# Optimization experiments

Hardware: AMD Instinct MI355X
Metric: run time of the kernel (lower is better)

The kernel has to match this reference:

```python
import jax, jax.numpy as jnp
import numpy as np
from jax import lax

LEADS = 61
BETA = 2.0
DN = ('NCHW', 'OIHW', 'NCHW')


def setup_inputs() -> dict:
    key = jax.random.key(0)
    ks = jax.random.split(key, 11)
    B, L = 128, LEADS
    w = lambda k, shape: jax.random.normal(k, shape, jnp.float32) * 0.1
    return {
        "x": jax.random.normal(ks[0], (B, L, 32, 250), jnp.float32),
        "w1": w(ks[1], (L, 8, 1, 3, 4)),   "b1": w(ks[2], (L, 8)),
        "w2": w(ks[3], (L, 16, 8, 4, 3)),  "b2": w(ks[4], (L, 16)),
        "w3": w(ks[5], (L, 32, 16, 3, 4)), "b3": w(ks[6], (L, 32)),
        "w4": w(ks[7], (L, 64, 32, 2, 4)), "b4": w(ks[8], (L, 64)),
        "fcw": w(ks[9], (L, 3, 64)),       "fcb": w(ks[10], (L, 3)),
    }


def _maxpool2(h):
    return lax.reduce_window(h, -jnp.inf, lax.max, (1, 1, 2, 2), (1, 1, 2, 2), 'VALID')


def _lead(x, w1, b1, w2, b2, w3, b3, w4, b4, fcw, fcb):
    # x: (B,1,32,250) for a single lead; weights for that lead only
    h = lax.conv_general_dilated(x, w1, (1, 2), [(1, 1), (2, 2)], dimension_numbers=DN) + b1[None, :, None, None]
    h = jax.nn.relu(_maxpool2(h))                                  # (B,8,16,63)
    h = lax.conv_general_dilated(h, w2, (2, 2), [(1, 1), (1, 1)], dimension_numbers=DN) + b2[None, :, None, None]
    h = jax.nn.relu(_maxpool2(h))                                  # (B,16,4,16)
    h = lax.conv_general_dilated(h, w3, (1, 2), [(1, 1), (1, 1)], dimension_numbers=DN) + b3[None, :, None, None]
    h = jax.nn.relu(_maxpool2(h))                                  # (B,32,2,4)
    h = lax.conv_general_dilated(h, w4, (1, 1), 'VALID', dimension_numbers=DN) + b4[None, :, None, None]  # (B,64,1,1)
    h = h.reshape(h.shape[0], 64)
    logits = h @ fcw.T + fcb                                       # (B,3)
    return jax.nn.softmax(logits, axis=-1)


def reference(x, w1, b1, w2, b2, w3, b3, w4, b4, fcw, fcb):
    # batch all 61 per-lead pipelines via vmap over the lead axis
    xl = jnp.transpose(x, (1, 0, 2, 3))[:, :, None]                # (L,B,1,32,250)
    preds = jax.vmap(_lead)(xl, w1, b1, w2, b2, w3, b3, w4, b4, fcw, fcb)  # (L,B,3)
    preds = jnp.transpose(preds, (1, 0, 2))                        # (B,L,3)
    # eval-mode multiplicative fusion loss (Liu et al.)
    one_m = 1.0 - preds
    prod_all = jnp.prod(one_m, axis=1, keepdims=True)              # prod over all leads
    coeff = lax.stop_gradient(prod_all / one_m)                    # prod over k != j (detached)
    beta_exp = BETA / (LEADS - 1)
    loss = -jnp.sum(coeff ** beta_exp * jnp.log(preds), axis=1)    # (B,3)
    return loss
```

## Files before the change

kernel.cpp:

```cpp
#include <hip/hip_runtime.h>
#include <math.h>
#include <utility>

#define NLEADS 61
#define AIL __attribute__((always_inline))

template <int... Is, typename F>
__device__ __forceinline__ void sf_(std::integer_sequence<int, Is...>, F&& f) {
    (f(std::integral_constant<int, Is>{}), ...);
}
template <int N, typename F>
__device__ __forceinline__ void static_for(F&& f) {
    sf_(std::make_integer_sequence<int, N>{}, (F&&)f);
}

__device__ __forceinline__ float4 ld4(const float* p) { return *(const float4*)p; }
__device__ __forceinline__ float2 ld2(const float* p) { return *(const float2*)p; }

template <int C> __device__ __forceinline__ float f4c(float4 v) {
    if constexpr (C == 0) return v.x;
    else if constexpr (C == 1) return v.y;
    else if constexpr (C == 2) return v.z;
    else return v.w;
}
template <int C> __device__ __forceinline__ float f6(float4 a, float2 b) {
    if constexpr (C < 4) return f4c<C>(a);
    else if constexpr (C == 4) return b.x;
    else return b.y;
}
template <int K> __device__ __forceinline__ float w12(float4 w0, float4 w1, float4 w2) {
    if constexpr (K < 4) return f4c<K>(w0);
    else if constexpr (K < 8) return f4c<K - 4>(w1);
    else return f4c<K - 8>(w2);
}

__global__ __launch_bounds__(256, 4)
void lead_cnn_kernel(const float* __restrict__ x,
                     const float* __restrict__ w1g, const float* __restrict__ b1g,
                     const float* __restrict__ w2g, const float* __restrict__ b2g,
                     const float* __restrict__ w3g, const float* __restrict__ b3g,
                     const float* __restrict__ w4g, const float* __restrict__ b4g,
                     const float* __restrict__ fcwg, const float* __restrict__ fcbg,
                     float* __restrict__ preds)
{
    __shared__ __align__(16) float smem[9992];
    float* const A  = smem;
    float* const H2 = smem + 8704;

    const int t = threadIdx.x;
    const int b = blockIdx.x;
    const int l = blockIdx.y;

    const float* xg  = x + ((size_t)b * NLEADS + l) * 8000;
    const float* w1l = w1g + l * 96;
    const float* b1l = b1g + l * 8;

    float acc1[32];
    static_for<4>([&](auto IT) AIL {
        constexpr int it = IT.value;
        const int item = t + it * 256;
        const int ph = item / 63;
        const int pw = item - ph * 63;
        const int c1 = (pw == 0) ? 0 : (4 * pw - 2);
        const int c3 = (pw >= 62) ? 248 : (4 * pw + 2);
        const bool lok = (pw > 0), rok = (pw < 62);
        float xw[24];
        static_for<4>([&](auto R) AIL {
            constexpr int r = R.value;
            const int ih = 2 * ph - 1 + r;
            const int rr = (ih < 0) ? 0 : ((ih > 31) ? 31 : ih);
            const bool rowok = ((unsigned)ih < 32u);
            const float* xr = xg + rr * 250;
            const float2 e0 = ld2(xr + c1);
            const float2 e1 = ld2(xr + 4 * pw);
            const float2 e2 = ld2(xr + c3);
            const bool okl = rowok & lok, okr = rowok & rok;
            xw[r*6+0] = okl ? e0.x : 0.f;
            xw[r*6+1] = okl ? e0.y : 0.f;
            xw[r*6+2] = rowok ? e1.x : 0.f;
            xw[r*6+3] = rowok ? e1.y : 0.f;
            xw[r*6+4] = okr ? e2.x : 0.f;
            xw[r*6+5] = okr ? e2.y : 0.f;
        });
        static_for<8>([&](auto OC) AIL {
            constexpr int oc = OC.value;
            const float4 q0 = ld4(w1l + oc * 12);
            const float4 q1 = ld4(w1l + oc * 12 + 4);
            const float4 q2 = ld4(w1l + oc * 12 + 8);
            float p00 = 0.f, p01 = 0.f, p10 = 0.f, p11 = 0.f;
            static_for<3>([&](auto KH) AIL {
                constexpr int kh = KH.value;
                static_for<4>([&](auto KW) AIL {
                    constexpr int kw = KW.value;
                    const float wv = w12<kh * 4 + kw>(q0, q1, q2);
                    p00 = fmaf(wv, xw[kh * 6 + kw], p00);
                    p01 = fmaf(wv, xw[kh * 6 + kw + 2], p01);
                    p10 = fmaf(wv, xw[(kh + 1) * 6 + kw], p10);
                    p11 = fmaf(wv, xw[(kh + 1) * 6 + kw + 2], p11);
                });
            });
            const float m = fmaxf(fmaxf(p00, p01), fmaxf(p10, p11));
            acc1[it * 8 + oc] = fmaxf(m + b1l[oc], 0.f);
        });
    });
    static_for<4>([&](auto IT) AIL {
        constexpr int it = IT.value;
        const int item = t + it * 256;
        if (item < 1008) {
            const int ph = item / 63;
            const int pw = item - ph * 63;
            const int base = ph * 68 + pw + 1;
            static_for<8>([&](auto OC) AIL {
                A[OC.value * 1088 + base] = acc1[it * 8 + OC.value];
            });
        }
    });
    for (int i = t; i < 640; i += 256) {
        const int ch = i / 80, j = i - ch * 80;
        const int r = j / 5, k = j - r * 5;
        A[ch * 1088 + r * 68 + ((k == 0) ? 0 : (63 + k))] = 0.f;
    }
    for (int i = t; i < 128; i += 256) {
        const int ch = i >> 3, r = (i >> 1) & 3;
        H2[ch * 80 + r * 20 + ((i & 1) ? 17 : 0)] = 0.f;
    }
    __syncthreads();

    {
        const int s2 = t & 63;
        const int ogu = __builtin_amdgcn_readfirstlane(t >> 6);
        const int ph2 = s2 >> 4, pw2 = s2 & 15;
        float a2[16];
        static_for<16>([&](auto I) AIL { a2[I.value] = 0.f; });
        static_for<8>([&](auto IC) AIL {
            constexpr int ic = IC.value;
            float4 ya[6]; float2 yb[6];
            static_for<6>([&](auto R) AIL {
                constexpr int r = R.value;
                const int Rr = 4 * ph2 - 1 + r;
                const int rr = (Rr < 0) ? 0 : ((Rr > 15) ? 15 : Rr);
                const float* hp = A + ic * 1088 + rr * 68 + 4 * pw2;
                float4 va = ld4(hp);
                float2 vb = ld2(hp + 4);
                if constexpr (r == 0 || r == 5) {
                    const bool ok = ((unsigned)Rr < 16u);
                    va.x = ok ? va.x : 0.f; va.y = ok ? va.y : 0.f;
                    va.z = ok ? va.z : 0.f; va.w = ok ? va.w : 0.f;
                    vb.x = ok ? vb.x : 0.f; vb.y = ok ? vb.y : 0.f;
                }
                ya[r] = va; yb[r] = vb;
            });
            static_for<4>([&](auto OL) AIL {
                constexpr int ol = OL.value;
                const float* wp = w2g + ((size_t)((l * 16 + ogu * 4 + ol) * 8 + ic)) * 12;
                const float4 q0 = ld4(wp), q1 = ld4(wp + 4), q2 = ld4(wp + 8);
                static_for<4>([&](auto KH) AIL {
                    constexpr int kh = KH.value;
                    static_for<3>([&](auto KW) AIL {
                        constexpr int kw = KW.value;
                        const float wv = w12<kh * 3 + kw>(q0, q1, q2);
                        a2[ol*4+0] = fmaf(wv, f6<kw>(ya[kh], yb[kh]), a2[ol*4+0]);
                        a2[ol*4+1] = fmaf(wv, f6<kw + 2>(ya[kh], yb[kh]), a2[ol*4+1]);
                        a2[ol*4+2] = fmaf(wv, f6<kw>(ya[kh + 2], yb[kh + 2]), a2[ol*4+2]);
                        a2[ol*4+3] = fmaf(wv, f6<kw + 2>(ya[kh + 2], yb[kh + 2]), a2[ol*4+3]);
                    });
                });
            });
        });
        static_for<4>([&](auto OL) AIL {
            constexpr int ol = OL.value;
            const int oc = ogu * 4 + ol;
            const float m = fmaxf(fmaxf(a2[ol*4+0], a2[ol*4+1]),
                                  fmaxf(a2[ol*4+2], a2[ol*4+3]));
            H2[oc * 80 + ph2 * 20 + pw2 + 1] = fmaxf(m + b2g[l * 16 + oc], 0.f);
        });
    }
    __syncthreads();

    {
        const int oc3 = t >> 3, s3 = t & 7;
        const int ph3 = s3 >> 2, pw3 = s3 & 3;
        const float* w3l = w3g + (size_t)l * 6144 + oc3 * 192;
        const float b3v = b3g[l * 32 + oc3];
        float a30 = 0.f, a31 = 0.f, a32 = 0.f, a33 = 0.f;
        static_for<16>([&](auto IC) AIL {
            constexpr int ic = IC.value;
            float4 za[4]; float2 zb[4];
            static_for<4>([&](auto R) AIL {
                constexpr int r = R.value;
                const int Rr = 2 * ph3 - 1 + r;
                const int rr = (Rr < 0) ? 0 : ((Rr > 3) ? 3 : Rr);
                const float* zp = H2 + ic * 80 + rr * 20 + 4 * pw3;
                float4 va = ld4(zp);
                float2 vb = ld2(zp + 4);
                if constexpr (r == 0 || r == 3) {
                    const bool ok = ((unsigned)Rr < 4u);
                    va.x = ok ? va.x : 0.f; va.y = ok ? va.y : 0.f;
                    va.z = ok ? va.z : 0.f; va.w = ok ? va.w : 0.f;
                    vb.x = ok ? vb.x : 0.f; vb.y = ok ? vb.y : 0.f;
                }
                za[r] = va; zb[r] = vb;
            });
            const float4 q0 = ld4(w3l + ic * 12);
            const float4 q1 = ld4(w3l + ic * 12 + 4);
            const float4 q2 = ld4(w3l + ic * 12 + 8);
            static_for<3>([&](auto KH) AIL {
                constexpr int kh = KH.value;
                static_for<4>([&](auto KW) AIL {
                    constexpr int kw = KW.value;
                    const float wv = w12<kh * 4 + kw>(q0, q1, q2);
                    a30 = fmaf(wv, f6<kw>(za[kh], zb[kh]), a30);
                    a31 = fmaf(wv, f6<kw + 2>(za[kh], zb[kh]), a31);
                    a32 = fmaf(wv, f6<kw>(za[kh + 1], zb[kh + 1]), a32);
                    a33 = fmaf(wv, f6<kw + 2>(za[kh + 1], zb[kh + 1]), a33);
                });
            });
        });
        const float m = fmaxf(fmaxf(a30, a31), fmaxf(a32, a33));
        A[oc3 * 8 + s3] = fmaxf(m + b3v, 0.f);
    }
    __syncthreads();

    {
        if (t < 192) A[600 + t] = fcwg[l * 192 + t];
        else if (t < 195) A[600 + t] = fcbg[l * 3 + (t - 192)];

        const int oc4 = t >> 2, part = t & 3;
        const float* w4p = w4g + (size_t)l * 16384 + oc4 * 256 + part * 64;
        float s4 = 0.f;
        static_for<8>([&](auto J) AIL {
            constexpr int j = J.value;
            const float4 wa = ld4(w4p + j * 8);
            const float4 wb = ld4(w4p + j * 8 + 4);
            const float* xx = A + (part * 8 + j) * 8;
            const float4 xA = ld4(xx), xB = ld4(xx + 4);
            s4 = fmaf(wa.x, xA.x, s4); s4 = fmaf(wa.y, xA.y, s4);
            s4 = fmaf(wa.z, xA.z, s4); s4 = fmaf(wa.w, xA.w, s4);
            s4 = fmaf(wb.x, xB.x, s4); s4 = fmaf(wb.y, xB.y, s4);
            s4 = fmaf(wb.z, xB.z, s4); s4 = fmaf(wb.w, xB.w, s4);
        });
        A[256 + part * 64 + oc4] = s4;
    }
    __syncthreads();
    if (t < 64)
        A[512 + t] = A[256 + t] + A[320 + t] + A[384 + t] + A[448 + t]
                   + b4g[l * 64 + t];
    __syncthreads();

    if (t < 3) {
        float s = A[792 + t];
        static_for<64>([&](auto I) AIL {
            s = fmaf(A[600 + t * 64 + I.value], A[512 + I.value], s);
        });
        A[580 + t] = s;
    }
    __syncthreads();
    if (t == 0) {
        const float a0 = A[580], a1 = A[581], a2 = A[582];
        const float m = fmaxf(a0, fmaxf(a1, a2));
        const float e0 = expf(a0 - m), e1 = expf(a1 - m), e2 = expf(a2 - m);
        const float inv = 1.f / (e0 + e1 + e2);
        float* pr = preds + ((size_t)b * NLEADS + l) * 3;
        pr[0] = e0 * inv; pr[1] = e1 * inv; pr[2] = e2 * inv;
    }
}

__global__ void fusion_loss_kernel(const float* __restrict__ preds,
                                   float* __restrict__ out, int B)
{
    const int idx = blockIdx.x * blockDim.x + threadIdx.x;
    if (idx >= B * 3) return;
    const int b = idx / 3;
    const int c = idx - 3 * b;
    const float* p = preds + (size_t)b * (NLEADS * 3) + c;
    float S = 0.f;
    for (int j = 0; j < NLEADS; ++j) S += logf(1.f - p[j * 3]);
    const float be = 2.0f / 60.0f;
    float loss = 0.f;
    for (int j = 0; j < NLEADS; ++j) {
        const float pj = p[j * 3];
        loss += expf(be * (S - logf(1.f - pj))) * logf(pj);
    }
    out[idx] = -loss;
}

extern "C" void kernel_launch(void* const* d_in, const int* in_sizes, int n_in,
                              void* d_out, int out_size, void* d_ws, size_t ws_size,
                              hipStream_t stream)
{
    const float* x   = (const float*)d_in[0];
    const float* w1  = (const float*)d_in[1];
    const float* b1  = (const float*)d_in[2];
    const float* w2  = (const float*)d_in[3];
    const float* b2  = (const float*)d_in[4];
    const float* w3  = (const float*)d_in[5];
    const float* b3  = (const float*)d_in[6];
    const float* w4  = (const float*)d_in[7];
    const float* b4  = (const float*)d_in[8];
    const float* fcw = (const float*)d_in[9];
    const float* fcb = (const float*)d_in[10];

    const int B = in_sizes[0] / (NLEADS * 32 * 250);
    float* preds = (float*)d_ws;

    dim3 grid(B, NLEADS);
    hipLaunchKernelGGL(lead_cnn_kernel, grid, dim3(256), 0, stream,
                       x, w1, b1, w2, b2, w3, b3, w4, b4, fcw, fcb, preds);

    const int total = B * 3;
    hipLaunchKernelGGL(fusion_loss_kernel, dim3((total + 255) / 256), dim3(256),
                       0, stream, preds, (float*)d_out, B);
}
```

Measured before the change: 559.7 us.

## Halve conv1 LDS staging by splitting conv2 over two channel halves

```diff
diff --git a/kernel.cpp b/kernel.cpp
--- a/kernel.cpp
+++ b/kernel.cpp
@@ -34,7 +34,7 @@
     else return f4c<K - 8>(w2);
 }
 
-__global__ __launch_bounds__(256, 4)
+__global__ __launch_bounds__(256, 6)
 void lead_cnn_kernel(const float* __restrict__ x,
                      const float* __restrict__ w1g, const float* __restrict__ b1g,
                      const float* __restrict__ w2g, const float* __restrict__ b2g,
@@ -43,9 +43,9 @@
                      const float* __restrict__ fcwg, const float* __restrict__ fcbg,
                      float* __restrict__ preds)
 {
-    __shared__ __align__(16) float smem[9992];
+    __shared__ __align__(16) float smem[5640];
     float* const A  = smem;
-    float* const H2 = smem + 8704;
+    float* const H2 = smem + 4352;
 
     const int t = threadIdx.x;
     const int b = blockIdx.x;
@@ -55,15 +55,29 @@
     const float* w1l = w1g + l * 96;
     const float* b1l = b1g + l * 8;
 
+    if (t < 192) {
+        const int ic = t / 48, j = t - ic * 48;
+        const int r = j / 3, k = j - r * 3;
+        A[ic * 1088 + r * 68 + ((k == 0) ? 0 : (63 + k))] = 0.f;
+    }
+    if (t >= 128) {
+        const int i = t - 128;
+        const int ch = i >> 3, r = (i >> 1) & 3;
+        H2[ch * 80 + r * 20 + ((i & 1) ? 17 : 0)] = 0.f;
+    }
+
+    const int pw = t & 63;
+    const int rg = t >> 6;
+    const int cm = (pw <= 62) ? 4 * pw : 248;
+    const int c1 = (pw == 0) ? 0 : ((pw <= 62) ? 4 * pw - 2 : 248);
+    const int c3 = (pw >= 62) ? 248 : 4 * pw + 2;
+    const bool lok = (pw > 0);
+    const bool rok = (pw < 62);
+
     float acc1[32];
     static_for<4>([&](auto IT) AIL {
         constexpr int it = IT.value;
-        const int item = t + it * 256;
-        const int ph = item / 63;
-        const int pw = item - ph * 63;
-        const int c1 = (pw == 0) ? 0 : (4 * pw - 2);
-        const int c3 = (pw >= 62) ? 248 : (4 * pw + 2);
-        const bool lok = (pw > 0), rok = (pw < 62);
+        const int ph = rg * 4 + it;
         float xw[24];
         static_for<4>([&](auto R) AIL {
             constexpr int r = R.value;
@@ -72,7 +86,7 @@
             const bool rowok = ((unsigned)ih < 32u);
             const float* xr = xg + rr * 250;
             const float2 e0 = ld2(xr + c1);
-            const float2 e1 = ld2(xr + 4 * pw);
+            const float2 e1 = ld2(xr + cm);
             const float2 e2 = ld2(xr + c3);
             const bool okl = rowok & lok, okr = rowok & rok;
             xw[r*6+0] = okl ? e0.x : 0.f;
@@ -103,43 +117,32 @@
             acc1[it * 8 + oc] = fmaxf(m + b1l[oc], 0.f);
         });
     });
-    static_for<4>([&](auto IT) AIL {
-        constexpr int it = IT.value;
-        const int item = t + it * 256;
-        if (item < 1008) {
-            const int ph = item / 63;
-            const int pw = item - ph * 63;
-            const int base = ph * 68 + pw + 1;
-            static_for<8>([&](auto OC) AIL {
-                A[OC.value * 1088 + base] = acc1[it * 8 + OC.value];
-            });
-        }
-    });
-    for (int i = t; i < 640; i += 256) {
-        const int ch = i / 80, j = i - ch * 80;
-        const int r = j / 5, k = j - r * 5;
-        A[ch * 1088 + r * 68 + ((k == 0) ? 0 : (63 + k))] = 0.f;
-    }
-    for (int i = t; i < 128; i += 256) {
-        const int ch = i >> 3, r = (i >> 1) & 3;
-        H2[ch * 80 + r * 20 + ((i & 1) ? 17 : 0)] = 0.f;
-    }
-    __syncthreads();
-
-    {
-        const int s2 = t & 63;
-        const int ogu = __builtin_amdgcn_readfirstlane(t >> 6);
-        const int ph2 = s2 >> 4, pw2 = s2 & 15;
-        float a2[16];
-        static_for<16>([&](auto I) AIL { a2[I.value] = 0.f; });
-        static_for<8>([&](auto IC) AIL {
-            constexpr int ic = IC.value;
+
+    if (pw < 63) {
+        static_for<4>([&](auto IT) AIL {
+            const int base = (rg * 4 + IT.value) * 68 + pw + 1;
+            static_for<4>([&](auto OC) AIL {
+                A[OC.value * 1088 + base] = acc1[IT.value * 8 + OC.value];
+            });
+        });
+    }
+    __syncthreads();
+
+    const int s2 = t & 63;
+    const int ogu = __builtin_amdgcn_readfirstlane(t >> 6);
+    const int ph2 = s2 >> 4, pw2 = s2 & 15;
+    float a2[16];
+    static_for<16>([&](auto I) AIL { a2[I.value] = 0.f; });
+
+    auto conv2_half = [&](int wic0) AIL {
+        static_for<4>([&](auto ICL) AIL {
+            constexpr int icl = ICL.value;
             float4 ya[6]; float2 yb[6];
             static_for<6>([&](auto R) AIL {
                 constexpr int r = R.value;
                 const int Rr = 4 * ph2 - 1 + r;
                 const int rr = (Rr < 0) ? 0 : ((Rr > 15) ? 15 : Rr);
-                const float* hp = A + ic * 1088 + rr * 68 + 4 * pw2;
+                const float* hp = A + icl * 1088 + rr * 68 + 4 * pw2;
                 float4 va = ld4(hp);
                 float2 vb = ld2(hp + 4);
                 if constexpr (r == 0 || r == 5) {
@@ -152,7 +155,8 @@
             });
             static_for<4>([&](auto OL) AIL {
                 constexpr int ol = OL.value;
-                const float* wp = w2g + ((size_t)((l * 16 + ogu * 4 + ol) * 8 + ic)) * 12;
+                const float* wp = w2g
+                    + ((size_t)((l * 16 + ogu * 4 + ol) * 8 + wic0 + icl)) * 12;
                 const float4 q0 = ld4(wp), q1 = ld4(wp + 4), q2 = ld4(wp + 8);
                 static_for<4>([&](auto KH) AIL {
                     constexpr int kh = KH.value;
@@ -167,14 +171,29 @@
                 });
             });
         });
-        static_for<4>([&](auto OL) AIL {
-            constexpr int ol = OL.value;
-            const int oc = ogu * 4 + ol;
-            const float m = fmaxf(fmaxf(a2[ol*4+0], a2[ol*4+1]),
-                                  fmaxf(a2[ol*4+2], a2[ol*4+3]));
-            H2[oc * 80 + ph2 * 20 + pw2 + 1] = fmaxf(m + b2g[l * 16 + oc], 0.f);
-        });
-    }
+    };
+
+    conv2_half(0);
+    __syncthreads();
+
+    if (pw < 63) {
+        static_for<4>([&](auto IT) AIL {
+            const int base = (rg * 4 + IT.value) * 68 + pw + 1;
+            static_for<4>([&](auto OC) AIL {
+                A[OC.value * 1088 + base] = acc1[IT.value * 8 + 4 + OC.value];
+            });
+        });
+    }
+    __syncthreads();
+
+    conv2_half(4);
+    static_for<4>([&](auto OL) AIL {
+        constexpr int ol = OL.value;
+        const int oc = ogu * 4 + ol;
+        const float m = fmaxf(fmaxf(a2[ol*4+0], a2[ol*4+1]),
+                              fmaxf(a2[ol*4+2], a2[ol*4+3]));
+        H2[oc * 80 + ph2 * 20 + pw2 + 1] = fmaxf(m + b2g[l * 16 + oc], 0.f);
+    });
     __syncthreads();
 
     {
@@ -256,9 +275,9 @@
     }
     __syncthreads();
     if (t == 0) {
-        const float a0 = A[580], a1 = A[581], a2 = A[582];
-        const float m = fmaxf(a0, fmaxf(a1, a2));
-        const float e0 = expf(a0 - m), e1 = expf(a1 - m), e2 = expf(a2 - m);
+        const float a0 = A[580], a1 = A[581], a2v = A[582];
+        const float m = fmaxf(a0, fmaxf(a1, a2v));
+        const float e0 = expf(a0 - m), e1 = expf(a1 - m), e2 = expf(a2v - m);
         const float inv = 1.f / (e0 + e1 + e2);
         float* pr = preds + ((size_t)b * NLEADS + l) * 3;
         pr[0] = e0 * inv; pr[1] = e1 * inv; pr[2] = e2 * inv;
```

After: 653.6 us. 16.8% more time.
